# Performance work log

Hardware: AMD Instinct MI355X
Metric: run time of the kernel (lower is better)

## Reference

```python
import jax, jax.numpy as jnp
import numpy as np

N_NODES = 50000
N_EDGES = 800000
IN_DIM = 128
HID_DIM = 128
OUT_DIM = 128
THRESH = 0.05
SCALE = 50.0
EPS = 1e-6


def _graph_conv(src, dst, feat, W, b):
    """DGL GraphConv with norm='both': D_out^{-1/2} -> sum-aggregate -> D_in^{-1/2} -> linear."""
    N = feat.shape[0]
    ones = jnp.ones(src.shape[0], feat.dtype)
    deg_out = jax.ops.segment_sum(ones, src, num_segments=N)
    deg_in = jax.ops.segment_sum(ones, dst, num_segments=N)
    norm_src = jax.lax.rsqrt(jnp.maximum(deg_out, 1.0))
    norm_dst = jax.lax.rsqrt(jnp.maximum(deg_in, 1.0))
    h = feat * norm_src[:, None]                       # [N, d]
    agg = jax.ops.segment_sum(h[src], dst, num_segments=N)  # SpMM: gather + scatter-add
    return (agg * norm_dst[:, None]) @ W + b


def _gnn(src, dst, x, W1, b1, W2, b2):
    h = jax.nn.relu(_graph_conv(src, dst, x, W1, b1))
    return _graph_conv(src, dst, h, W2, b2)


def _corr(z1, z2):
    # torch .std uses ddof=1 (unbiased)
    z1s = (z1 - z1.mean(axis=0)) / (jnp.std(z1, axis=0, ddof=1) + EPS)
    z2s = (z2 - z2.mean(axis=0)) / (jnp.std(z2, axis=0, ddof=1) + EPS)
    return (z1s.T @ z2s) / z1.shape[0]


def setup_inputs() -> dict:
    key = jax.random.key(0)
    ks = jax.random.split(key, 8)
    x1 = jax.random.normal(ks[0], (N_NODES, IN_DIM), jnp.float32)
    x2 = jax.random.normal(ks[1], (N_NODES, IN_DIM), jnp.float32)
    src1 = jax.random.randint(ks[2], (N_EDGES,), 0, N_NODES, jnp.int32)
    dst1 = jax.random.randint(ks[3], (N_EDGES,), 0, N_NODES, jnp.int32)
    src2 = jax.random.randint(ks[4], (N_EDGES,), 0, N_NODES, jnp.int32)
    dst2 = jax.random.randint(ks[5], (N_EDGES,), 0, N_NODES, jnp.int32)
    W1 = jax.random.normal(ks[6], (IN_DIM, HID_DIM), jnp.float32) / np.sqrt(IN_DIM)
    W2 = jax.random.normal(ks[7], (HID_DIM, OUT_DIM), jnp.float32) / np.sqrt(HID_DIM)
    return {
        "x1": x1, "x2": x2,
        "src1": src1, "dst1": dst1, "src2": src2, "dst2": dst2,
        "W1": W1, "b1": jnp.zeros((HID_DIM,), jnp.float32),
        "W2": W2, "b2": jnp.zeros((OUT_DIM,), jnp.float32),
        "row_offsets": jnp.zeros((OUT_DIM,), jnp.float32),
        "col_offsets": jnp.zeros((OUT_DIM,), jnp.float32),
    }


def reference(x1, x2, src1, dst1, src2, dst2, W1, b1, W2, b2, row_offsets, col_offsets):
    z1 = _gnn(src1, dst1, x1, W1, b1, W2, b2)
    z2 = _gnn(src2, dst2, x2, W1, b1, W2, b2)
    C = _corr(z1, z2)                                  # [D, D]
    row_score = jnp.abs(C).mean(axis=1)
    col_score = jnp.abs(C).mean(axis=0)
    row_mask = jax.nn.sigmoid(SCALE * (row_score + row_offsets - THRESH))
    col_mask = jax.nn.sigmoid(SCALE * (col_score + col_offsets - THRESH))
    C_masked = C * (row_mask[:, None] * col_mask[None, :])
    return (C_masked, row_mask, col_mask, z1, z2)
```

## Files before the change

### kernel.cpp

```cpp
#include <hip/hip_runtime.h>

#define D 128
#define THRESH 0.05f
#define SCALE 50.0f
#define EPS 1e-6f
#define GP 480
#define PGRP 30
#define CAP 60
#define PS 2
#define NRANGE 4
#define BB 48
#define RMAX 12500
#define RNGP 12512

typedef __attribute__((ext_vector_type(4))) int i4v;
typedef __attribute__((ext_vector_type(4))) float f4v;
typedef _Float16 h8v __attribute__((ext_vector_type(8)));

__device__ inline float4 ntload4(const float* p) {
    f4v v = __builtin_nontemporal_load((const f4v*)p);
    return make_float4(v.x, v.y, v.z, v.w);
}

__device__ inline void decode_grq(int bid, int& g, int& r, int& q) {
    g = bid >= (NRANGE * BB);
    int rem = g ? bid - NRANGE * BB : bid;
    r = rem & (NRANGE - 1);
    q = rem >> 2;
}

__global__ void __launch_bounds__(256) count_kernel(const int* __restrict__ src1,
                                                    const int* __restrict__ dst1,
                                                    const int* __restrict__ src2,
                                                    const int* __restrict__ dst2,
                                                    unsigned int* __restrict__ staging,
                                                    int E, int N) {
    __shared__ unsigned int cnt[RMAX];
    int g, r, q;
    decode_grq(blockIdx.x, g, r, q);
    const int* __restrict__ src = g ? src2 : src1;
    const int* __restrict__ dst = g ? dst2 : dst1;

    int rng = (N + NRANGE - 1) / NRANGE;
    int lo = r * rng;
    int hi = min(N, lo + rng);
    int nr = hi - lo;
    int seg = (E + BB - 1) / BB;
    int s0 = q * seg;
    int s1 = min(E, s0 + seg);
    int tid = threadIdx.x;

    for (int i = tid; i < nr; i += 256) cnt[i] = 0u;
    __syncthreads();

    for (int e = s0 + tid * 4; e < s1; e += 1024) {
        int ss[4], dd[4];
        if (e + 4 <= s1) {
            i4v a = *(const i4v*)(src + e);
            i4v b = *(const i4v*)(dst + e);
            ss[0] = a.x; ss[1] = a.y; ss[2] = a.z; ss[3] = a.w;
            dd[0] = b.x; dd[1] = b.y; dd[2] = b.z; dd[3] = b.w;
        } else {
#pragma unroll
            for (int c = 0; c < 4; ++c) {
                int ee = e + c;
                ss[c] = (ee < s1) ? src[ee] : -1;
                dd[c] = (ee < s1) ? dst[ee] : -1;
            }
        }
#pragma unroll
        for (int c = 0; c < 4; ++c) {
            int s = ss[c], d = dd[c];
            if (s >= lo && s < hi) atomicAdd(&cnt[s - lo], 1u);
            if (d >= lo && d < hi) atomicAdd(&cnt[d - lo], 0x10000u);
        }
    }
    __syncthreads();

    unsigned int* row = staging + (size_t)(((g * NRANGE + r) * BB) + q) * RNGP;
    for (int i = tid; i < nr; i += 256) row[i] = cnt[i];
}

__global__ void scan_kernel(unsigned int* __restrict__ staging, int* __restrict__ pad1,
                            int* __restrict__ pad2, int N) {
    int t = blockIdx.x * 256 + threadIdx.x;
    if (t >= 2 * N) return;
    int g = t >= N;
    int d = g ? t - N : t;
    int rng = (N + NRANGE - 1) / NRANGE;
    int r = d / rng;
    int i = d - r * rng;
    int* __restrict__ pad = g ? pad2 : pad1;

    unsigned int* base = staging + (size_t)((g * NRANGE + r) * BB) * RNGP + i;
    unsigned int oc = 0, run = 0;
#pragma unroll 4
    for (int q = 0; q < BB; ++q) {
        unsigned int c = base[(size_t)q * RNGP];
        base[(size_t)q * RNGP] = run;
        oc += c & 0xFFFFu;
        run += c >> 16;
    }
    pad[d * PS] = (int)oc;
    pad[d * PS + 1] = (int)run;
}

__global__ void __launch_bounds__(256) place_kernel(const int* __restrict__ src1,
                                                    const int* __restrict__ dst1,
                                                    const int* __restrict__ src2,
                                                    const int* __restrict__ dst2,
                                                    const unsigned int* __restrict__ staging,
                                                    unsigned short* __restrict__ bucket1,
                                                    unsigned short* __restrict__ bucket2,
                                                    int E, int N) {
    __shared__ unsigned int cur[RMAX];
    int g, r, q;
    decode_grq(blockIdx.x, g, r, q);
    const int* __restrict__ src = g ? src2 : src1;
    const int* __restrict__ dst = g ? dst2 : dst1;
    unsigned short* __restrict__ bucket = g ? bucket2 : bucket1;

    int rng = (N + NRANGE - 1) / NRANGE;
    int lo = r * rng;
    int hi = min(N, lo + rng);
    int nr = hi - lo;
    int seg = (E + BB - 1) / BB;
    int s0 = q * seg;
    int s1 = min(E, s0 + seg);
    int tid = threadIdx.x;

    const unsigned int* row = staging + (size_t)(((g * NRANGE + r) * BB) + q) * RNGP;
    for (int i = tid; i < nr; i += 256) cur[i] = row[i];
    __syncthreads();

    for (int e = s0 + tid * 4; e < s1; e += 1024) {
        int ss[4], dd[4];
        if (e + 4 <= s1) {
            i4v a = *(const i4v*)(src + e);
            i4v b = *(const i4v*)(dst + e);
            ss[0] = a.x; ss[1] = a.y; ss[2] = a.z; ss[3] = a.w;
            dd[0] = b.x; dd[1] = b.y; dd[2] = b.z; dd[3] = b.w;
        } else {
#pragma unroll
            for (int c = 0; c < 4; ++c) {
                int ee = e + c;
                ss[c] = (ee < s1) ? src[ee] : -1;
                dd[c] = (ee < s1) ? dst[ee] : -1;
            }
        }
#pragma unroll
        for (int c = 0; c < 4; ++c) {
            int s = ss[c], d = dd[c];
            if (d >= lo && d < hi) {
                unsigned int pos = atomicAdd(&cur[d - lo], 1u);
                if (pos < CAP) bucket[(size_t)d * CAP + pos] = (unsigned short)s;
            }
        }
    }
}

__global__ void wtrans_kernel(const float* __restrict__ W1, const float* __restrict__ W2,
                              _Float16* __restrict__ Wt1, _Float16* __restrict__ Wt2) {
    int e = blockIdx.x * 256 + threadIdx.x;
    int h = e >= D * D;
    int rem = h ? e - D * D : e;
    int j = rem >> 7, k = rem & 127;
    const float* W = h ? W2 : W1;
    _Float16* Wt = h ? Wt2 : Wt1;
    Wt[j * D + k] = (_Float16)W[k * D + j];
}

template <bool F32IN>
__global__ void __launch_bounds__(256) gemm_ns(const float* __restrict__ tf,
                                               const _Float16* __restrict__ th,
                                               const int* __restrict__ pad,
                                               const _Float16* __restrict__ Wt,
                                               _Float16* __restrict__ y, int N) {
    __shared__ _Float16 sA[128 * D];
    __shared__ _Float16 sB[D * D];
    int tid = threadIdx.x;
    int row0 = blockIdx.x * 128;

#pragma unroll
    for (int q = 0; q < 8; ++q) {
        int c = q * 256 + tid;
        int j = c >> 4, u = c & 15;
        h8v v = *(const h8v*)(Wt + j * D + u * 8);
        int byte = j * 256 + ((u * 16) ^ ((j & 7) << 4));
        *(h8v*)((char*)sB + byte) = v;
    }
#pragma unroll
    for (int q = 0; q < 8; ++q) {
        int c = q * 256 + tid;
        int row = c >> 4, u = c & 15;
        int gr = row0 + row;
        h8v hv = {};
        if (gr < N) {
            if (F32IN) {
                float nsv = rsqrtf(fmaxf((float)pad[gr * PS], 1.f));
                const float* p = tf + (size_t)gr * D + u * 8;
                float4 v0 = *(const float4*)p;
                float4 v1 = *(const float4*)(p + 4);
                hv[0] = (_Float16)(v0.x * nsv); hv[1] = (_Float16)(v0.y * nsv);
                hv[2] = (_Float16)(v0.z * nsv); hv[3] = (_Float16)(v0.w * nsv);
                hv[4] = (_Float16)(v1.x * nsv); hv[5] = (_Float16)(v1.y * nsv);
                hv[6] = (_Float16)(v1.z * nsv); hv[7] = (_Float16)(v1.w * nsv);
            } else {
                hv = *(const h8v*)(th + (size_t)gr * D + u * 8);
            }
        }
        int byte = row * 256 + ((u * 16) ^ ((row & 7) << 4));
        *(h8v*)((char*)sA + byte) = hv;
    }
    __syncthreads();

    int w = tid >> 6;
    int l = tid & 63;
    int l16 = l & 15, lg = l >> 4;
    f4v acc[2][8];
#pragma unroll
    for (int m = 0; m < 2; ++m)
#pragma unroll
        for (int n = 0; n < 8; ++n) acc[m][n] = (f4v){0.f, 0.f, 0.f, 0.f};

#pragma unroll
    for (int kc = 0; kc < 4; ++kc) {
        h8v a[2];
#pragma unroll
        for (int m = 0; m < 2; ++m) {
            int row = w * 32 + m * 16 + l16;
            int u = kc * 4 + lg;
            int byte = row * 256 + ((u * 16) ^ ((row & 7) << 4));
            a[m] = *(const h8v*)((const char*)sA + byte);
        }
#pragma unroll
        for (int n = 0; n < 8; ++n) {
            int j = n * 16 + l16;
            int u = kc * 4 + lg;
            int byte = j * 256 + ((u * 16) ^ ((j & 7) << 4));
            h8v b = *(const h8v*)((const char*)sB + byte);
#pragma unroll
            for (int m = 0; m < 2; ++m)
                acc[m][n] = __builtin_amdgcn_mfma_f32_16x16x32_f16(a[m], b, acc[m][n], 0, 0, 0);
        }
    }

#pragma unroll
    for (int m = 0; m < 2; ++m) {
        int rbase = row0 + w * 32 + m * 16 + lg * 4;
#pragma unroll
        for (int n = 0; n < 8; ++n) {
            int col = n * 16 + l16;
#pragma unroll
            for (int r = 0; r < 4; ++r) {
                int row = rbase + r;
                if (row < N) y[(size_t)row * D + col] = (_Float16)acc[m][n][r];
            }
        }
    }
}

template <bool OUT16>
__global__ void gather_kernel(const unsigned short* __restrict__ bucket,
                              const int* __restrict__ pad, const _Float16* __restrict__ y,
                              const float* __restrict__ bias, float* __restrict__ zf,
                              _Float16* __restrict__ zh, int N) {
    int wave = threadIdx.x >> 6;
    int lane = threadIdx.x & 63;
    int node = blockIdx.x * 4 + wave;
    if (node >= N) return;
    int deg = pad[node * PS + 1];
    int cnt = min(deg, CAP);
    float ndv = rsqrtf(fmaxf((float)deg, 1.f));
    int sid = 0;
    if (lane < cnt) sid = bucket[(size_t)node * CAP + lane];
    int grp = lane >> 4;
    int sl = lane & 15;
    const _Float16* yp = y + sl * 8;
    float acc[8] = {0.f, 0.f, 0.f, 0.f, 0.f, 0.f, 0.f, 0.f};
    for (int j = 0; j < cnt; j += 16) {
        h8v v[4];
        float vw[4];
#pragma unroll
        for (int c = 0; c < 4; ++c) {
            int idx = j + c * 4 + grp;
            int s = __shfl(sid, idx & 63);
            vw[c] = (idx < cnt) ? 1.f : 0.f;
            v[c] = *(const h8v*)(yp + (size_t)s * D);
        }
#pragma unroll
        for (int c = 0; c < 4; ++c)
#pragma unroll
            for (int u = 0; u < 8; ++u)
                acc[u] += (float)v[c][u] * vw[c];
    }
#pragma unroll
    for (int u = 0; u < 8; ++u) {
        acc[u] += __shfl_xor(acc[u], 16);
        acc[u] += __shfl_xor(acc[u], 32);
    }
    if (grp == 0) {
        float4 b0 = *(const float4*)(bias + sl * 8);
        float4 b1 = *(const float4*)(bias + sl * 8 + 4);
        float o[8];
        o[0] = acc[0] * ndv + b0.x; o[1] = acc[1] * ndv + b0.y;
        o[2] = acc[2] * ndv + b0.z; o[3] = acc[3] * ndv + b0.w;
        o[4] = acc[4] * ndv + b1.x; o[5] = acc[5] * ndv + b1.y;
        o[6] = acc[6] * ndv + b1.z; o[7] = acc[7] * ndv + b1.w;
        if (OUT16) {
            float nsv = rsqrtf(fmaxf((float)pad[node * PS], 1.f));
            h8v hv;
#pragma unroll
            for (int u = 0; u < 8; ++u) hv[u] = (_Float16)(fmaxf(o[u], 0.f) * nsv);
            *(h8v*)(zh + (size_t)node * D + sl * 8) = hv;
        } else {
            *(float4*)(zf + (size_t)node * D + sl * 8) = make_float4(o[0], o[1], o[2], o[3]);
            *(float4*)(zf + (size_t)node * D + sl * 8 + 4) = make_float4(o[4], o[5], o[6], o[7]);
        }
    }
}

__global__ void __launch_bounds__(512) gram_kernel(const float* __restrict__ z1,
                                                   const float* __restrict__ z2,
                                                   float* __restrict__ part,
                                                   float* __restrict__ stats, int N) {
    __shared__ float s1[16][D], s2[16][D];
    int tid = threadIdx.x;
    int ti = tid >> 4;
    int tj = tid & 15;
    float acc[4][8];
#pragma unroll
    for (int u = 0; u < 4; ++u)
#pragma unroll
        for (int v = 0; v < 8; ++v) acc[u][v] = 0.f;
    float ssum = 0.f, ssq = 0.f;
    int rpb = (N + GP - 1) / GP;
    int r0 = blockIdx.x * rpb;
    int r1 = min(N, r0 + rpb);
    for (int r = r0; r < r1; r += 16) {
#pragma unroll
        for (int q = 0; q < 2; ++q) {
            int idx = q * 512 + tid;
            int half = idx >> 9;
            int rem = idx & 511;
            int rr = rem >> 5, cc = (rem & 31) * 4;
            int row = r + rr;
            float4 v = make_float4(0.f, 0.f, 0.f, 0.f);
            const float* zp = half ? z2 : z1;
            if (row < r1) v = ntload4(&zp[(size_t)row * D + cc]);
            if (half) *(float4*)&s2[rr][cc] = v;
            else      *(float4*)&s1[rr][cc] = v;
        }
        __syncthreads();
        if (tid < 256) {
            const float* sc = (tid < 128) ? &s1[0][0] : &s2[0][0];
            int j = tid & 127;
#pragma unroll
            for (int q = 0; q < 16; ++q) {
                float v = sc[q * D + j];
                ssum += v;
                ssq += v * v;
            }
        }
#pragma unroll
        for (int q = 0; q < 16; ++q) {
            float4 a0 = *(const float4*)&s1[q][ti * 4];
            float4 b0 = *(const float4*)&s2[q][tj * 8];
            float4 b1 = *(const float4*)&s2[q][tj * 8 + 4];
            float a[4] = {a0.x, a0.y, a0.z, a0.w};
            float b[8] = {b0.x, b0.y, b0.z, b0.w, b1.x, b1.y, b1.z, b1.w};
#pragma unroll
            for (int u = 0; u < 4; ++u)
#pragma unroll
                for (int v = 0; v < 8; ++v) acc[u][v] += a[u] * b[v];
        }
        __syncthreads();
    }
    float* pb = part + (size_t)blockIdx.x * (D * D);
#pragma unroll
    for (int u = 0; u < 4; ++u) {
        *(float4*)&pb[(ti * 4 + u) * D + tj * 8] =
            make_float4(acc[u][0], acc[u][1], acc[u][2], acc[u][3]);
        *(float4*)&pb[(ti * 4 + u) * D + tj * 8 + 4] =
            make_float4(acc[u][4], acc[u][5], acc[u][6], acc[u][7]);
    }
    int j = tid & 127;
    if (tid < 128) {
        atomicAdd(&stats[j], ssum);
        atomicAdd(&stats[D + j], ssq);
    } else if (tid < 256) {
        atomicAdd(&stats[2 * D + j], ssum);
        atomicAdd(&stats[3 * D + j], ssq);
    }
}

__global__ void reduce_part(const float* __restrict__ part, float* __restrict__ Csum) {
    int e = blockIdx.x * 256 + threadIdx.x;
    int p0 = blockIdx.y * PGRP;
    float s = 0.f;
#pragma unroll
    for (int p = 0; p < PGRP; ++p)
        s += __builtin_nontemporal_load(&part[(size_t)(p0 + p) * (D * D) + e]);
    atomicAdd(&Csum[e], s);
}

__global__ void __launch_bounds__(1024) corrmask_kernel(const float* __restrict__ Csum,
                                                        const float* __restrict__ stats,
                                                        const float* __restrict__ roff,
                                                        const float* __restrict__ coff,
                                                        float* __restrict__ out, int N) {
    __shared__ float cL[D * D];
    __shared__ float m1s[D], i1s[D], m2s[D], i2s[D];
    __shared__ float rowpart[D][2];
    __shared__ float colpart[8][D];
    __shared__ float rms[D], cms[D];
    int t = threadIdx.x;
    int j = t & 127, rg = t >> 7;
    float fn = (float)N;
    if (t < D) {
        float m1 = stats[t] / fn;
        float v1 = fmaxf((stats[D + t] - fn * m1 * m1) / (fn - 1.f), 0.f);
        m1s[t] = m1;
        i1s[t] = 1.f / (sqrtf(v1) + EPS);
    } else if (t < 2 * D) {
        int jj = t - D;
        float m2 = stats[2 * D + jj] / fn;
        float v2 = fmaxf((stats[3 * D + jj] - fn * m2 * m2) / (fn - 1.f), 0.f);
        m2s[jj] = m2;
        i2s[jj] = 1.f / (sqrtf(v2) + EPS);
    }
    __syncthreads();
    float b = m2s[j], vj = i2s[j];
    float invfn = 1.f / fn;
    float colacc = 0.f;
    for (int k = 0; k < 16; ++k) {
        int i = rg * 16 + k;
        int e = i * D + j;
        float c = (Csum[e] - fn * m1s[i] * b) * (i1s[i] * vj) * invfn;
        cL[e] = c;
        float a = fabsf(c);
        colacc += a;
        for (int o = 1; o < 64; o <<= 1) a += __shfl_xor(a, o);
        if ((j & 63) == 0) rowpart[i][j >> 6] = a;
    }
    colpart[rg][j] = colacc;
    __syncthreads();
    if (t < D) {
        float rs = rowpart[t][0] + rowpart[t][1];
        float rm = 1.f / (1.f + expf(-SCALE * (rs / (float)D + roff[t] - THRESH)));
        rms[t] = rm;
        out[D * D + t] = rm;
    } else if (t < 2 * D) {
        int jj = t - D;
        float cs = 0.f;
#pragma unroll
        for (int g2 = 0; g2 < 8; ++g2) cs += colpart[g2][jj];
        float cm = 1.f / (1.f + expf(-SCALE * (cs / (float)D + coff[jj] - THRESH)));
        cms[jj] = cm;
        out[D * D + D + jj] = cm;
    }
    __syncthreads();
    for (int k = 0; k < 16; ++k) {
        int i = rg * 16 + k;
        int e = i * D + j;
        out[e] = cL[e] * rms[i] * cms[j];
    }
}

extern "C" void kernel_launch(void* const* d_in, const int* in_sizes, int n_in,
                              void* d_out, int out_size, void* d_ws, size_t ws_size,
                              hipStream_t stream) {
    const float* x1 = (const float*)d_in[0];
    const float* x2 = (const float*)d_in[1];
    const int* src1 = (const int*)d_in[2];
    const int* dst1 = (const int*)d_in[3];
    const int* src2 = (const int*)d_in[4];
    const int* dst2 = (const int*)d_in[5];
    const float* W1 = (const float*)d_in[6];
    const float* b1 = (const float*)d_in[7];
    const float* W2 = (const float*)d_in[8];
    const float* b2 = (const float*)d_in[9];
    const float* roff = (const float*)d_in[10];
    const float* coff = (const float*)d_in[11];

    const int N = in_sizes[0] / D;
    const int E = in_sizes[2];

    float* ws = (float*)d_ws;
    unsigned int* staging = (unsigned int*)ws;
    _Float16* y = (_Float16*)ws;
    unsigned short* bucket1 =
        (unsigned short*)(staging + (size_t)2 * NRANGE * BB * RNGP);
    unsigned short* bucket2 = bucket1 + (size_t)N * CAP;
    int* pad1 = (int*)(bucket2 + (size_t)N * CAP);
    int* pad2 = pad1 + (size_t)N * PS;
    _Float16* Wt1 = (_Float16*)(pad2 + (size_t)N * PS);
    _Float16* Wt2 = Wt1 + D * D;
    float* part = ws;
    float* stats = part + (size_t)GP * D * D;
    float* Csum = stats + 4 * D;

    float* out = (float*)d_out;
    float* z1 = out + D * D + 2 * D;
    float* z2 = z1 + (size_t)N * D;

    count_kernel<<<2 * NRANGE * BB, 256, 0, stream>>>(src1, dst1, src2, dst2, staging, E, N);
    scan_kernel<<<(2 * N + 255) / 256, 256, 0, stream>>>(staging, pad1, pad2, N);
    place_kernel<<<2 * NRANGE * BB, 256, 0, stream>>>(src1, dst1, src2, dst2, staging,
                                                      bucket1, bucket2, E, N);
    wtrans_kernel<<<2 * D * D / 256, 256, 0, stream>>>(W1, W2, Wt1, Wt2);

    const int gblk = (N + 127) / 128;
    for (int g = 0; g < 2; ++g) {
        const float* x = g ? x2 : x1;
        float* z = g ? z2 : z1;
        _Float16* hp = (_Float16*)z;
        int* pad = g ? pad2 : pad1;
        unsigned short* bucket = g ? bucket2 : bucket1;

        gemm_ns<true><<<gblk, 256, 0, stream>>>(x, nullptr, pad, Wt1, y, N);
        gather_kernel<true><<<(N + 3) / 4, 256, 0, stream>>>(bucket, pad, y, b1, nullptr, hp, N);
        gemm_ns<false><<<gblk, 256, 0, stream>>>(nullptr, hp, pad, Wt2, y, N);
        gather_kernel<false><<<(N + 3) / 4, 256, 0, stream>>>(bucket, pad, y, b2, z, nullptr, N);
    }

    hipMemsetAsync(stats, 0, sizeof(float) * (4 * D + D * D), stream);

    gram_kernel<<<GP, 512, 0, stream>>>(z1, z2, part, stats, N);
    {
        dim3 grid(64, GP / PGRP);
        reduce_part<<<grid, 256, 0, stream>>>(part, Csum);
    }
    corrmask_kernel<<<1, 1024, 0, stream>>>(Csum, stats, roff, coff, out, N);
}
```

Before: 280.7 us.

## Compute correlation Gram matrix with FP16 MFMA on transposed node-major inputs

Adds a kernel that converts z1/z2 to FP16 and transposes them to a feature-major padded layout. The FP32 shared-memory Gram kernel is replaced by one using 16x16x32 f16 MFMA instructions, with fewer blocks (96 instead of 480), which also shrinks the partial-sum reduction. Column sums and sums of squares are now computed from the FP16 values. This trades an extra transpose pass and reduced precision in the statistics and correlation for matrix-core throughput.

```diff
diff --git a/kernel.cpp b/kernel.cpp
--- a/kernel.cpp
+++ b/kernel.cpp
@@ -4,8 +4,10 @@
 #define THRESH 0.05f
 #define SCALE 50.0f
 #define EPS 1e-6f
-#define GP 480
-#define PGRP 30
+#define GP 96
+#define RPB 544
+#define NP2 52224
+#define PGRP 24
 #define CAP 60
 #define PS 2
 #define NRANGE 4
@@ -16,6 +18,7 @@
 typedef __attribute__((ext_vector_type(4))) int i4v;
 typedef __attribute__((ext_vector_type(4))) float f4v;
 typedef _Float16 h8v __attribute__((ext_vector_type(8)));
+typedef _Float16 h4v __attribute__((ext_vector_type(4)));
 
 __device__ inline float4 ntload4(const float* p) {
     f4v v = __builtin_nontemporal_load((const f4v*)p);
@@ -320,77 +323,90 @@
     }
 }
 
-__global__ void __launch_bounds__(512) gram_kernel(const float* __restrict__ z1,
-                                                   const float* __restrict__ z2,
-                                                   float* __restrict__ part,
-                                                   float* __restrict__ stats, int N) {
-    __shared__ float s1[16][D], s2[16][D];
+__global__ void __launch_bounds__(256) ztrans_kernel(const float* __restrict__ z1,
+                                                     const float* __restrict__ z2,
+                                                     _Float16* __restrict__ zt1,
+                                                     _Float16* __restrict__ zt2, int N) {
+    __shared__ _Float16 tile[64][132];
+    int g = blockIdx.y;
+    const float* z = g ? z2 : z1;
+    _Float16* zt = g ? zt2 : zt1;
+    int n0 = blockIdx.x * 64;
     int tid = threadIdx.x;
-    int ti = tid >> 4;
-    int tj = tid & 15;
-    float acc[4][8];
-#pragma unroll
-    for (int u = 0; u < 4; ++u)
-#pragma unroll
-        for (int v = 0; v < 8; ++v) acc[u][v] = 0.f;
-    float ssum = 0.f, ssq = 0.f;
-    int rpb = (N + GP - 1) / GP;
-    int r0 = blockIdx.x * rpb;
-    int r1 = min(N, r0 + rpb);
-    for (int r = r0; r < r1; r += 16) {
-#pragma unroll
-        for (int q = 0; q < 2; ++q) {
-            int idx = q * 512 + tid;
-            int half = idx >> 9;
-            int rem = idx & 511;
-            int rr = rem >> 5, cc = (rem & 31) * 4;
-            int row = r + rr;
-            float4 v = make_float4(0.f, 0.f, 0.f, 0.f);
-            const float* zp = half ? z2 : z1;
-            if (row < r1) v = ntload4(&zp[(size_t)row * D + cc]);
-            if (half) *(float4*)&s2[rr][cc] = v;
-            else      *(float4*)&s1[rr][cc] = v;
-        }
-        __syncthreads();
-        if (tid < 256) {
-            const float* sc = (tid < 128) ? &s1[0][0] : &s2[0][0];
-            int j = tid & 127;
-#pragma unroll
-            for (int q = 0; q < 16; ++q) {
-                float v = sc[q * D + j];
-                ssum += v;
-                ssq += v * v;
+#pragma unroll
+    for (int it = 0; it < 8; ++it) {
+        int idx = it * 256 + tid;
+        int row = idx >> 5;
+        int c4 = (idx & 31) * 4;
+        int gr = n0 + row;
+        float4 v = make_float4(0.f, 0.f, 0.f, 0.f);
+        if (gr < N) v = *(const float4*)&z[(size_t)gr * D + c4];
+        h4v h = {(_Float16)v.x, (_Float16)v.y, (_Float16)v.z, (_Float16)v.w};
+        *(h4v*)&tile[row][c4] = h;
+    }
+    __syncthreads();
+    int col = tid >> 1, half = tid & 1;
+    _Float16 buf[32];
+#pragma unroll
+    for (int k = 0; k < 32; ++k) buf[k] = tile[half * 32 + k][col];
+    _Float16* dst = zt + (size_t)col * NP2 + n0 + half * 32;
+#pragma unroll
+    for (int c = 0; c < 4; ++c) *(h8v*)(dst + c * 8) = *(const h8v*)&buf[c * 8];
+}
+
+__global__ void __launch_bounds__(512) gram_mfma(const _Float16* __restrict__ zt1,
+                                                 const _Float16* __restrict__ zt2,
+                                                 float* __restrict__ part,
+                                                 float* __restrict__ stats) {
+    int tid = threadIdx.x;
+    int w = tid >> 6, l = tid & 63;
+    int l16 = l & 15, lg = l >> 4;
+    f4v acc[8];
+#pragma unroll
+    for (int n = 0; n < 8; ++n) acc[n] = (f4v){0.f, 0.f, 0.f, 0.f};
+    float sA = 0.f, qA = 0.f, sB = 0.f, qB = 0.f;
+    int r0 = blockIdx.x * RPB;
+    const _Float16* ap = zt1 + (size_t)(w * 16 + l16) * NP2 + lg * 8;
+#pragma unroll 1
+    for (int ks = 0; ks < RPB / 32; ++ks) {
+        int k0 = r0 + ks * 32;
+        h8v a = *(const h8v*)(ap + k0);
+#pragma unroll
+        for (int j = 0; j < 8; ++j) {
+            float f = (float)a[j];
+            sA += f;
+            qA += f * f;
+        }
+#pragma unroll
+        for (int n = 0; n < 8; ++n) {
+            h8v b = *(const h8v*)(zt2 + (size_t)(n * 16 + l16) * NP2 + k0 + lg * 8);
+            if (n == w) {
+#pragma unroll
+                for (int j = 0; j < 8; ++j) {
+                    float f = (float)b[j];
+                    sB += f;
+                    qB += f * f;
+                }
             }
-        }
-#pragma unroll
-        for (int q = 0; q < 16; ++q) {
-            float4 a0 = *(const float4*)&s1[q][ti * 4];
-            float4 b0 = *(const float4*)&s2[q][tj * 8];
-            float4 b1 = *(const float4*)&s2[q][tj * 8 + 4];
-            float a[4] = {a0.x, a0.y, a0.z, a0.w};
-            float b[8] = {b0.x, b0.y, b0.z, b0.w, b1.x, b1.y, b1.z, b1.w};
-#pragma unroll
-            for (int u = 0; u < 4; ++u)
-#pragma unroll
-                for (int v = 0; v < 8; ++v) acc[u][v] += a[u] * b[v];
-        }
-        __syncthreads();
+            acc[n] = __builtin_amdgcn_mfma_f32_16x16x32_f16(a, b, acc[n], 0, 0, 0);
+        }
     }
     float* pb = part + (size_t)blockIdx.x * (D * D);
 #pragma unroll
-    for (int u = 0; u < 4; ++u) {
-        *(float4*)&pb[(ti * 4 + u) * D + tj * 8] =
-            make_float4(acc[u][0], acc[u][1], acc[u][2], acc[u][3]);
-        *(float4*)&pb[(ti * 4 + u) * D + tj * 8 + 4] =
-            make_float4(acc[u][4], acc[u][5], acc[u][6], acc[u][7]);
-    }
-    int j = tid & 127;
-    if (tid < 128) {
-        atomicAdd(&stats[j], ssum);
-        atomicAdd(&stats[D + j], ssq);
-    } else if (tid < 256) {
-        atomicAdd(&stats[2 * D + j], ssum);
-        atomicAdd(&stats[3 * D + j], ssq);
+    for (int n = 0; n < 8; ++n)
+#pragma unroll
+        for (int r = 0; r < 4; ++r)
+            pb[(w * 16 + lg * 4 + r) * D + n * 16 + l16] = acc[n][r];
+    sA += __shfl_xor(sA, 16); sA += __shfl_xor(sA, 32);
+    qA += __shfl_xor(qA, 16); qA += __shfl_xor(qA, 32);
+    sB += __shfl_xor(sB, 16); sB += __shfl_xor(sB, 32);
+    qB += __shfl_xor(qB, 16); qB += __shfl_xor(qB, 32);
+    if (lg == 0) {
+        int row = w * 16 + l16;
+        atomicAdd(&stats[row], sA);
+        atomicAdd(&stats[D + row], qA);
+        atomicAdd(&stats[2 * D + row], sB);
+        atomicAdd(&stats[3 * D + row], qB);
     }
 }
 
@@ -496,7 +512,9 @@
     int* pad2 = pad1 + (size_t)N * PS;
     _Float16* Wt1 = (_Float16*)(pad2 + (size_t)N * PS);
     _Float16* Wt2 = Wt1 + D * D;
-    float* part = ws;
+    _Float16* zt1 = (_Float16*)ws;
+    _Float16* zt2 = zt1 + (size_t)D * NP2;
+    float* part = (float*)(zt2 + (size_t)D * NP2);
     float* stats = part + (size_t)GP * D * D;
     float* Csum = stats + 4 * D;
 
@@ -525,8 +543,11 @@
     }
 
     hipMemsetAsync(stats, 0, sizeof(float) * (4 * D + D * D), stream);
-
-    gram_kernel<<<GP, 512, 0, stream>>>(z1, z2, part, stats, N);
+    {
+        dim3 tgrid(NP2 / 64, 2);
+        ztrans_kernel<<<tgrid, 256, 0, stream>>>(z1, z2, zt1, zt2, N);
+    }
+    gram_mfma<<<GP, 512, 0, stream>>>(zt1, zt2, part, stats);
     {
         dim3 grid(64, GP / PGRP);
         reduce_part<<<grid, 256, 0, stream>>>(part, Csum);
```

Result: slower. 292.5 us (+4.2%).
